# Kernel optimization log

Measured on AMD Instinct MI355X. Metric: run time of the kernel, lower is better.

The kernel has to match this reference:

```python
import jax, jax.numpy as jnp
import numpy as np

B, SX, SL, D, H = 4, 4096, 256, 1024, 16
DH = D // H
LN_EPS = 1e-5
RMS_EPS = 1e-8


def layernorm(x, g, b):
    mu = jnp.mean(x, axis=-1, keepdims=True)
    var = jnp.mean(jnp.square(x - mu), axis=-1, keepdims=True)
    return (x - mu) * jax.lax.rsqrt(var + LN_EPS) * g + b


def rmsnorm(x, gamma):
    # torch: norm = ||x||_2 * dim^-0.5 ; x / clamp(norm, eps) * gamma
    norm = jnp.sqrt(jnp.sum(jnp.square(x), axis=-1, keepdims=True)) * (DH ** -0.5)
    return x / jnp.maximum(norm, RMS_EPS) * gamma


def setup_inputs() -> dict:
    key = jax.random.key(0)
    ks = jax.random.split(key, 6)
    s = 0.02
    return {
        "x": jax.random.normal(ks[0], (B, SX, D), jnp.float32),
        "latents": jax.random.normal(ks[1], (B, SL, D), jnp.float32),
        "mask_x": jnp.ones((B, SX), jnp.float32),
        "mask_latent": jnp.ones((B, SL), jnp.float32),
        "ln_x_g": jnp.ones((D,), jnp.float32),
        "ln_x_b": jnp.zeros((D,), jnp.float32),
        "ln_l_g": jnp.ones((D,), jnp.float32),
        "ln_l_b": jnp.zeros((D,), jnp.float32),
        "Wq": jax.random.normal(ks[2], (D, D), jnp.float32) * s,
        "Wkv": jax.random.normal(ks[3], (D, 2 * D), jnp.float32) * s,
        "qk_gamma": jnp.ones((DH,), jnp.float32),
        "Wo": jax.random.normal(ks[4], (D, D), jnp.float32) * s,
    }


def reference(x, latents, mask_x, mask_latent, ln_x_g, ln_x_b, ln_l_g, ln_l_b, Wq, Wkv, qk_gamma, Wo):
    xn = layernorm(x, ln_x_g, ln_x_b)                       # [B,SX,D]
    ln = layernorm(latents, ln_l_g, ln_l_b)                 # [B,SL,D]

    q = (ln @ Wq).reshape(B, SL, H, DH).transpose(0, 2, 1, 3)      # [B,H,SL,DH]
    kv_in = jnp.concatenate([xn, ln], axis=1)                      # [B,SX+SL,D]
    kv = kv_in @ Wkv
    Skv = SX + SL
    k = kv[..., :D].reshape(B, Skv, H, DH).transpose(0, 2, 1, 3)   # [B,H,Skv,DH]
    v = kv[..., D:].reshape(B, Skv, H, DH).transpose(0, 2, 1, 3)

    # NOTE: original code applies query_norm to BOTH q and k (faithful to source)
    q = rmsnorm(q, qk_gamma)
    k = rmsnorm(k, qk_gamma)

    scores = jnp.einsum("bhqd,bhkd->bhqk", q, k) / np.sqrt(DH)     # [B,H,SL,Skv]

    kv_mask = jnp.concatenate([mask_x, mask_latent], axis=1)       # [B,Skv]
    mask = kv_mask[:, None, :] * mask_latent[:, :, None]           # [B,SL,Skv]
    add_mask = (1.0 - mask)[:, None, :, :] * jnp.finfo(scores.dtype).min
    attn = jax.nn.softmax(scores + add_mask, axis=-1)

    y = jnp.einsum("bhqk,bhkd->bhqd", attn, v)                     # [B,H,SL,DH]
    y = y.transpose(0, 2, 1, 3).reshape(B, SL, D)
    return y @ Wo
```

## Files before the change

### kernel.cpp

```cpp
#include <hip/hip_runtime.h>

#define NB   4
#define SXX  4096
#define SLL  256
#define DD   1024
#define HH   16
#define DHH  64
#define SKV  4352
#define MKV  17408
#define NSPLIT 8

typedef __attribute__((ext_vector_type(8))) short bfrag;
typedef __attribute__((ext_vector_type(4))) float facc;

__device__ __forceinline__ unsigned short f2bf(float f){
  unsigned u = __builtin_bit_cast(unsigned, f);
  u = (u + 0x7fffu + ((u >> 16) & 1u)) >> 16;
  return (unsigned short)u;
}
__device__ __forceinline__ float bf2f(unsigned short h){
  unsigned u = ((unsigned)h) << 16;
  return __builtin_bit_cast(float, u);
}

#define GLOAD_LDS16(g, lds) __builtin_amdgcn_global_load_lds( \
    (const __attribute__((address_space(1))) unsigned int*)(const void*)(g), \
    (__attribute__((address_space(3))) unsigned int*)(void*)(lds), 16, 0, 0)

__global__ void wtrans3(const float* __restrict__ Wq, const float* __restrict__ Wkv,
                        const float* __restrict__ Wo, unsigned short* __restrict__ wqt,
                        unsigned short* __restrict__ wkvt, unsigned short* __restrict__ wot){
  __shared__ float t[32][33];
  int z = blockIdx.z;
  const float* in; unsigned short* out; int N;
  if (z == 0){ in = Wq;  out = wqt;  N = DD;   }
  else if (z == 1){ in = Wkv; out = wkvt; N = 2*DD; }
  else { in = Wo;  out = wot;  N = DD;   }
  int n0 = blockIdx.x * 32, k0 = blockIdx.y * 32;
  if (n0 >= N) return;
  int tx = threadIdx.x, ty = threadIdx.y;
  #pragma unroll
  for (int i = 0; i < 4; i++)
    t[ty + 8*i][tx] = in[(size_t)(k0 + ty + 8*i) * N + n0 + tx];
  __syncthreads();
  #pragma unroll
  for (int i = 0; i < 4; i++)
    out[(size_t)(n0 + ty + 8*i) * DD + k0 + tx] = f2bf(t[tx][ty + 8*i]);
}

__global__ void lnorm(const float* __restrict__ src, const float* __restrict__ g,
                      const float* __restrict__ bt, unsigned short* __restrict__ kvin,
                      unsigned short* __restrict__ dst2, int seq, int off){
  int row = blockIdx.x;
  int b = row / seq, s = row - b*seq;
  int t = threadIdx.x;
  const float4* rp = (const float4*)(src + (size_t)row * DD);
  float4 v = rp[t];
  float sum = v.x + v.y + v.z + v.w;
  float sq  = v.x*v.x + v.y*v.y + v.z*v.z + v.w*v.w;
  #pragma unroll
  for (int o = 32; o > 0; o >>= 1){ sum += __shfl_down(sum, o); sq += __shfl_down(sq, o); }
  __shared__ float ls[8];
  int w = t >> 6, l = t & 63;
  if (l == 0){ ls[w] = sum; ls[4 + w] = sq; }
  __syncthreads();
  sum = ls[0] + ls[1] + ls[2] + ls[3];
  sq  = ls[4] + ls[5] + ls[6] + ls[7];
  float mu  = sum * (1.f/DD);
  float var = sq * (1.f/DD) - mu*mu;
  float rs  = rsqrtf(var + 1e-5f);
  float4 gv = ((const float4*)g)[t];
  float4 bv = ((const float4*)bt)[t];
  ushort4 o4;
  o4.x = f2bf((v.x - mu)*rs*gv.x + bv.x);
  o4.y = f2bf((v.y - mu)*rs*gv.y + bv.y);
  o4.z = f2bf((v.z - mu)*rs*gv.z + bv.z);
  o4.w = f2bf((v.w - mu)*rs*gv.w + bv.w);
  *(ushort4*)(kvin + (size_t)(b*SKV + off + s) * DD + t*4) = o4;
  if (dst2) *(ushort4*)(dst2 + (size_t)row * DD + t*4) = o4;
}

__global__ __launch_bounds__(256) void gemm64(const unsigned short* __restrict__ A,
    const unsigned short* __restrict__ Bt, int M, int N, int K, float* __restrict__ outF){
  __shared__ unsigned short lA[64][72];
  __shared__ unsigned short lB[64][72];
  int n0 = blockIdx.x * 64, m0 = blockIdx.y * 64;
  int t = threadIdx.x, w = t >> 6, l = t & 63;
  int wr = (w >> 1) * 32, wc = (w & 1) * 32;
  int lr = l & 15, kq = (l >> 4) * 8;
  facc acc00 = (facc)0.f, acc01 = (facc)0.f, acc10 = (facc)0.f, acc11 = (facc)0.f;
  for (int k0 = 0; k0 < K; k0 += 64){
    #pragma unroll
    for (int cc = 0; cc < 2; cc++){
      int ch = t + cc*256;
      int row = ch >> 3, cg = (ch & 7) * 8;
      *(bfrag*)&lA[row][cg] = *(const bfrag*)&A[(size_t)(m0 + row) * K + k0 + cg];
      *(bfrag*)&lB[row][cg] = *(const bfrag*)&Bt[(size_t)(n0 + row) * K + k0 + cg];
    }
    __syncthreads();
    #pragma unroll
    for (int ks = 0; ks < 2; ks++){
      bfrag a0 = *(const bfrag*)&lA[wr + lr][ks*32 + kq];
      bfrag a1 = *(const bfrag*)&lA[wr + 16 + lr][ks*32 + kq];
      bfrag b0 = *(const bfrag*)&lB[wc + lr][ks*32 + kq];
      bfrag b1 = *(const bfrag*)&lB[wc + 16 + lr][ks*32 + kq];
      acc00 = __builtin_amdgcn_mfma_f32_16x16x32_bf16(a0, b0, acc00, 0, 0, 0);
      acc01 = __builtin_amdgcn_mfma_f32_16x16x32_bf16(a0, b1, acc01, 0, 0, 0);
      acc10 = __builtin_amdgcn_mfma_f32_16x16x32_bf16(a1, b0, acc10, 0, 0, 0);
      acc11 = __builtin_amdgcn_mfma_f32_16x16x32_bf16(a1, b1, acc11, 0, 0, 0);
    }
    __syncthreads();
  }
  int rl = (l >> 4) * 4, cl = l & 15;
  facc accs[2][2] = {{acc00, acc01},{acc10, acc11}};
  #pragma unroll
  for (int mt = 0; mt < 2; mt++)
  #pragma unroll
  for (int nt = 0; nt < 2; nt++)
  #pragma unroll
  for (int j = 0; j < 4; j++){
    int r = m0 + wr + mt*16 + rl + j;
    int c = n0 + wc + nt*16 + cl;
    outF[(size_t)r * N + c] = accs[mt][nt][j];
  }
}

__global__ __launch_bounds__(256) void gemm_q(const unsigned short* __restrict__ A,
    const unsigned short* __restrict__ Bt, const float* __restrict__ gamma,
    unsigned short* __restrict__ qn){
  __shared__ char smemb[18432];
  unsigned short* lA = (unsigned short*)smemb;
  unsigned short* lB = lA + 64*72;
  float* Cf = (float*)smemb;
  int h = blockIdx.x, n0 = h * 64, m0 = blockIdx.y * 64;
  int t = threadIdx.x, w = t >> 6, l = t & 63;
  int wr = (w >> 1) * 32, wc = (w & 1) * 32;
  int lr = l & 15, kq = (l >> 4) * 8;
  facc acc00 = (facc)0.f, acc01 = (facc)0.f, acc10 = (facc)0.f, acc11 = (facc)0.f;
  for (int k0 = 0; k0 < 1024; k0 += 64){
    #pragma unroll
    for (int cc = 0; cc < 2; cc++){
      int ch = t + cc*256;
      int row = ch >> 3, cg = (ch & 7) * 8;
      *(bfrag*)&lA[row*72 + cg] = *(const bfrag*)&A[(size_t)(m0 + row) * 1024 + k0 + cg];
      *(bfrag*)&lB[row*72 + cg] = *(const bfrag*)&Bt[(size_t)(n0 + row) * 1024 + k0 + cg];
    }
    __syncthreads();
    #pragma unroll
    for (int ks = 0; ks < 2; ks++){
      bfrag a0 = *(const bfrag*)&lA[(wr + lr)*72 + ks*32 + kq];
      bfrag a1 = *(const bfrag*)&lA[(wr + 16 + lr)*72 + ks*32 + kq];
      bfrag b0 = *(const bfrag*)&lB[(wc + lr)*72 + ks*32 + kq];
      bfrag b1 = *(const bfrag*)&lB[(wc + 16 + lr)*72 + ks*32 + kq];
      acc00 = __builtin_amdgcn_mfma_f32_16x16x32_bf16(a0, b0, acc00, 0, 0, 0);
      acc01 = __builtin_amdgcn_mfma_f32_16x16x32_bf16(a0, b1, acc01, 0, 0, 0);
      acc10 = __builtin_amdgcn_mfma_f32_16x16x32_bf16(a1, b0, acc10, 0, 0, 0);
      acc11 = __builtin_amdgcn_mfma_f32_16x16x32_bf16(a1, b1, acc11, 0, 0, 0);
    }
    __syncthreads();
  }
  int rl = (l >> 4) * 4, cl = l & 15;
  facc accs[2][2] = {{acc00, acc01},{acc10, acc11}};
  #pragma unroll
  for (int mt = 0; mt < 2; mt++)
  #pragma unroll
  for (int nt = 0; nt < 2; nt++)
  #pragma unroll
  for (int j = 0; j < 4; j++)
    Cf[(wr + mt*16 + rl + j)*66 + wc + nt*16 + cl] = accs[mt][nt][j];
  __syncthreads();
  if (t < 64){
    const float* src = &Cf[t*66];
    float ss = 0.f;
    #pragma unroll
    for (int d = 0; d < 64; d++){ float a = src[d]; ss = fmaf(a, a, ss); }
    float rv = 0.125f / fmaxf(sqrtf(ss) * 0.125f, 1e-8f);
    int r = m0 + t, b = r >> 8, sl = r & 255;
    unsigned short* dst = &qn[((size_t)(b*HH + h)*SLL + sl)*DHH];
    #pragma unroll
    for (int i = 0; i < 8; i++){
      ushort4 p; float g;
      g = gamma[i*8+0]; p.x = f2bf(src[i*8+0]*g*g*rv);
      g = gamma[i*8+1]; p.y = f2bf(src[i*8+1]*g*g*rv);
      g = gamma[i*8+2]; p.z = f2bf(src[i*8+2]*g*g*rv);
      g = gamma[i*8+3]; p.w = f2bf(src[i*8+3]*g*g*rv);
      ushort4 q;
      g = gamma[i*8+4]; q.x = f2bf(src[i*8+4]*g*g*rv);
      g = gamma[i*8+5]; q.y = f2bf(src[i*8+5]*g*g*rv);
      g = gamma[i*8+6]; q.z = f2bf(src[i*8+6]*g*g*rv);
      g = gamma[i*8+7]; q.w = f2bf(src[i*8+7]*g*g*rv);
      *(ushort4*)&dst[i*8]     = p;
      *(ushort4*)&dst[i*8 + 4] = q;
    }
  }
}

__global__ __launch_bounds__(512, 2) void gemm_kv(const unsigned short* __restrict__ A,
    const unsigned short* __restrict__ Bt,
    const float* __restrict__ mask_x, const float* __restrict__ mask_lat,
    unsigned short* __restrict__ outK, unsigned short* __restrict__ outV,
    float* __restrict__ rkm){
  __shared__ alignas(16) unsigned short lds[3 * 24576];
  int bid = blockIdx.x;
  int wg = (bid & 7) * 136 + (bid >> 3);
  int m0 = (wg >> 4) * 256, n0 = (wg & 15) * 128;
  int t = threadIdx.x, w = t >> 6, l = t & 63;
  int wm = w >> 1, wn = w & 1;
  int lr = l & 15, q2 = l >> 4;
  int r8 = l >> 3, u = l & 7;
  int swz = (u ^ (r8 & 7)) * 8;
  const unsigned short* Ag = A  + (size_t)(m0 + w*8 + r8) * 1024 + swz;
  const unsigned short* Bg = Bt + (size_t)(n0 + w*8 + r8) * 1024 + swz;

  facc acc[4][4];
  #pragma unroll
  for (int mt = 0; mt < 4; mt++)
  #pragma unroll
  for (int nt = 0; nt < 4; nt++) acc[mt][nt] = (facc)0.f;

#define SBAR __builtin_amdgcn_sched_barrier(0)
#define KV_BARRIER do { SBAR; __builtin_amdgcn_s_barrier(); SBAR; } while(0)
#define KV_STA(j, i) GLOAD_LDS16(Ag + (size_t)(i)*65536 + (j)*64, \
    &lds[((j) % 3)*24576 + (i)*4096 + w*512])
#define KV_STB(j, i) GLOAD_LDS16(Bg + (size_t)(i)*65536 + (j)*64, \
    &lds[((j) % 3)*24576 + 16384 + (i)*4096 + w*512])
#define KV_LDFRAG(j, ks) { \
    const unsigned short* pA = &lds[((j) % 3)*24576 + (wm*64 + lr)*64 + (((ks)*4 + q2) ^ (lr & 7))*8]; \
    const unsigned short* pB = &lds[((j) % 3)*24576 + 16384 + (wn*64 + lr)*64 + (((ks)*4 + q2) ^ (lr & 7))*8]; \
    av[0] = *(const bfrag*)(pA);        av[1] = *(const bfrag*)(pA + 1024); \
    av[2] = *(const bfrag*)(pA + 2048); av[3] = *(const bfrag*)(pA + 3072); \
    bv[0] = *(const bfrag*)(pB);        bv[1] = *(const bfrag*)(pB + 1024); \
    bv[2] = *(const bfrag*)(pB + 2048); bv[3] = *(const bfrag*)(pB + 3072); }
#define KV_MFMA do { \
    __builtin_amdgcn_s_setprio(1); \
    _Pragma("unroll") \
    for (int mt = 0; mt < 4; mt++){ \
      _Pragma("unroll") \
      for (int nt = 0; nt < 4; nt++) \
        acc[mt][nt] = __builtin_amdgcn_mfma_f32_16x16x32_bf16(av[mt], bv[nt], acc[mt][nt], 0, 0, 0); } \
    __builtin_amdgcn_s_setprio(0); } while(0)

  KV_STA(0,0); KV_STA(0,1); KV_STA(0,2); KV_STA(0,3); KV_STB(0,0); KV_STB(0,1);
  KV_STA(1,0); KV_STA(1,1); KV_STA(1,2); KV_STA(1,3); KV_STB(1,0); KV_STB(1,1);
  __asm__ volatile("s_waitcnt vmcnt(6)" ::: "memory");
  KV_BARRIER;

  bfrag av[4], bv[4];
  #pragma unroll
  for (int j = 0; j < 16; j++){
    KV_LDFRAG(j, 0);
    if (j < 14){ KV_STA(j+2, 0); KV_STA(j+2, 1); KV_STB(j+2, 0); }
    KV_BARRIER;
    KV_MFMA;
    KV_BARRIER;
    KV_LDFRAG(j, 1);
    if (j < 14){ KV_STA(j+2, 2); KV_STA(j+2, 3); KV_STB(j+2, 1); }
    KV_BARRIER;
    KV_MFMA;
    if (j < 14)       { __asm__ volatile("s_waitcnt vmcnt(6)" ::: "memory"); }
    else if (j == 14) { __asm__ volatile("s_waitcnt vmcnt(0)" ::: "memory"); }
    KV_BARRIER;
  }
#undef KV_STA
#undef KV_STB
#undef KV_LDFRAG
#undef KV_MFMA

  int b = m0 / SKV, s0 = m0 - b*SKV;
  if (n0 < DD){
    #pragma unroll
    for (int mt = 0; mt < 4; mt++)
    #pragma unroll
    for (int nt = 0; nt < 4; nt++)
    #pragma unroll
    for (int j = 0; j < 4; j++)
      lds[(wm*64 + mt*16 + q2*4 + j)*136 + wn*64 + nt*16 + lr] = f2bf(acc[mt][nt][j]);
    __syncthreads();
    int s = t >> 1, hf = t & 1;
    int srow = s0 + s;
    float cm = (srow < SXX) ? mask_x[b*SXX + srow] : mask_lat[b*SLL + srow - SXX];
    const unsigned short* src = &lds[s*136 + hf*64];
    uint4 wv[8];
    #pragma unroll
    for (int i = 0; i < 8; i++) wv[i] = *(const uint4*)&src[i*8];
    float ss0 = 0.f, ss1 = 0.f;
    #pragma unroll
    for (int i = 0; i < 8; i++){
      const unsigned short* pp = (const unsigned short*)&wv[i];
      #pragma unroll
      for (int e = 0; e < 4; e++){
        float a = bf2f(pp[e]);     ss0 = fmaf(a, a, ss0);
        float c = bf2f(pp[e + 4]); ss1 = fmaf(c, c, ss1);
      }
    }
    float rv = 1.f / fmaxf(sqrtf(ss0 + ss1) * 0.125f, 1e-8f);
    int h = (n0 >> 6) + hf;
    unsigned short* dst = &outK[((size_t)(b*HH + h)*SKV + srow)*DHH];
    #pragma unroll
    for (int i = 0; i < 8; i++)
      *(uint4*)&dst[i*8] = wv[i];
    rkm[((size_t)(b*HH + h))*SKV + srow] = (cm != 0.f) ? rv : -1.f;
  } else {
    #pragma unroll
    for (int mt = 0; mt < 4; mt++)
    #pragma unroll
    for (int nt = 0; nt < 4; nt++){
      ushort4 p;
      p.x = f2bf(acc[mt][nt][0]); p.y = f2bf(acc[mt][nt][1]);
      p.z = f2bf(acc[mt][nt][2]); p.w = f2bf(acc[mt][nt][3]);
      *(ushort4*)&lds[(wn*64 + nt*16 + lr)*264 + wm*64 + mt*16 + q2*4] = p;
    }
    __syncthreads();
    int c = t >> 2, sq = t & 3;
    int hh = ((n0 - DD) >> 6) + (c >> 6), d = c & 63;
    const unsigned short* src = &lds[c*264 + sq*64];
    unsigned short* dst = &outV[((size_t)(b*HH + hh)*DHH + d)*SKV + s0 + sq*64];
    #pragma unroll
    for (int i = 0; i < 8; i++)
      *(uint4*)&dst[i*8] = *(const uint4*)&src[i*8];
  }
}

__global__ __launch_bounds__(256) void attn(const unsigned short* __restrict__ qn,
    const unsigned short* __restrict__ kbuf, const unsigned short* __restrict__ vT,
    const float* __restrict__ rkm, const float* __restrict__ mask_lat,
    float* __restrict__ Opart, float* __restrict__ lpart){
  int qt = blockIdx.x, bh = blockIdx.y, split = blockIdx.z;
  int b = bh >> 4;
  __shared__ unsigned short lP[4][2][16][68];
  int t = threadIdx.x, w = t >> 6, l = t & 63;
  int lr = l & 15, q2 = l >> 4, kq = q2 * 8;
  int q0 = qt * 128;
  bfrag aq0[2], aq1[2];
  float rm[2][4];
  #pragma unroll
  for (int tt = 0; tt < 2; tt++){
    const unsigned short* qbase = qn + ((size_t)bh * SLL + q0 + tt*64 + w*16 + lr) * DHH;
    aq0[tt] = *(const bfrag*)&qbase[kq];
    aq1[tt] = *(const bfrag*)&qbase[32 + kq];
    #pragma unroll
    for (int j = 0; j < 4; j++) rm[tt][j] = mask_lat[b*SLL + q0 + tt*64 + w*16 + q2*4 + j];
  }
  facc O[2][4];
  #pragma unroll
  for (int tt = 0; tt < 2; tt++)
  #pragma unroll
  for (int nt = 0; nt < 4; nt++) O[tt][nt] = (facc)0.f;
  float lsum[2][4];
  #pragma unroll
  for (int tt = 0; tt < 2; tt++)
  #pragma unroll
  for (int j = 0; j < 4; j++) lsum[tt][j] = 0.f;

  int t0 = (split * 68) / NSPLIT, t1 = ((split + 1) * 68) / NSPLIT;
  for (int kt = t0; kt < t1; kt++){
    int key0 = kt * 64;
    const unsigned short* kb = kbuf + ((size_t)bh * SKV + key0) * DHH;
    bfrag bk0[4], bk1[4]; float rk[4];
    #pragma unroll
    for (int nt = 0; nt < 4; nt++){
      bk0[nt] = *(const bfrag*)&kb[(nt*16 + lr)*DHH + kq];
      bk1[nt] = *(const bfrag*)&kb[(nt*16 + lr)*DHH + 32 + kq];
      rk[nt]  = rkm[(size_t)bh*SKV + key0 + nt*16 + lr];
    }
    facc S[2][4];
    #pragma unroll
    for (int tt = 0; tt < 2; tt++)
    #pragma unroll
    for (int nt = 0; nt < 4; nt++){
      S[tt][nt] = (facc)0.f;
      S[tt][nt] = __builtin_amdgcn_mfma_f32_16x16x32_bf16(aq0[tt], bk0[nt], S[tt][nt], 0, 0, 0);
      S[tt][nt] = __builtin_amdgcn_mfma_f32_16x16x32_bf16(aq1[tt], bk1[nt], S[tt][nt], 0, 0, 0);
    }
    const unsigned short* vb = vT + (size_t)bh * DHH * SKV + key0;
    bfrag bv0[4], bv1[4];
    #pragma unroll
    for (int nt = 0; nt < 4; nt++){
      bv0[nt] = *(const bfrag*)&vb[(size_t)(nt*16 + lr)*SKV + kq];
      bv1[nt] = *(const bfrag*)&vb[(size_t)(nt*16 + lr)*SKV + 32 + kq];
    }
    #pragma unroll
    for (int tt = 0; tt < 2; tt++){
      #pragma unroll
      for (int j = 0; j < 4; j++){
        float rs_ = 0.f;
        #pragma unroll
        for (int nt = 0; nt < 4; nt++){
          float x = S[tt][nt][j] * rk[nt];
          float sv = (rk[nt] >= 0.f && rm[tt][j] != 0.f) ? x : -3.0e38f;
          float p = __expf(sv - 8.0f);
          rs_ += p;
          lP[w][tt][q2*4 + j][nt*16 + lr] = f2bf(p);
        }
        lsum[tt][j] += rs_;
      }
    }
    __asm__ volatile("s_waitcnt lgkmcnt(0)" ::: "memory");
    bfrag ap0[2], ap1[2];
    #pragma unroll
    for (int tt = 0; tt < 2; tt++){
      ap0[tt] = *(const bfrag*)&lP[w][tt][lr][kq];
      ap1[tt] = *(const bfrag*)&lP[w][tt][lr][32 + kq];
    }
    #pragma unroll
    for (int nt = 0; nt < 4; nt++){
      #pragma unroll
      for (int tt = 0; tt < 2; tt++){
        O[tt][nt] = __builtin_amdgcn_mfma_f32_16x16x32_bf16(ap0[tt], bv0[nt], O[tt][nt], 0, 0, 0);
        O[tt][nt] = __builtin_amdgcn_mfma_f32_16x16x32_bf16(ap1[tt], bv1[nt], O[tt][nt], 0, 0, 0);
      }
    }
  }
  #pragma unroll
  for (int tt = 0; tt < 2; tt++)
  #pragma unroll
  for (int j = 0; j < 4; j++){
    float L = lsum[tt][j];
    L += __shfl_xor(L, 1); L += __shfl_xor(L, 2);
    L += __shfl_xor(L, 4); L += __shfl_xor(L, 8);
    int srow = q0 + tt*64 + w*16 + q2*4 + j;
    size_t obase = (((size_t)split*64 + bh)*SLL + srow)*DHH;
    #pragma unroll
    for (int nt = 0; nt < 4; nt++)
      Opart[obase + nt*16 + lr] = O[tt][nt][j];
    if (lr == 0)
      lpart[((size_t)split*64 + bh)*SLL + srow] = L;
  }
}

__global__ __launch_bounds__(256) void attn_combine(const float* __restrict__ Opart,
    const float* __restrict__ lpart, unsigned short* __restrict__ ybuf){
  int t = threadIdx.x, w = t >> 6, l = t & 63;
  int idx = blockIdx.x * 4 + w;
  int bh = idx >> 8, srow = idx & 255;
  int b = bh >> 4, h = bh & 15;
  float L = 0.f, acc = 0.f;
  #pragma unroll
  for (int s = 0; s < NSPLIT; s++){
    L   += lpart[((size_t)s*64 + bh)*SLL + srow];
    acc += Opart[(((size_t)s*64 + bh)*SLL + srow)*DHH + l];
  }
  ybuf[((size_t)b*SLL + srow)*DD + h*DHH + l] = f2bf(acc / L);
}

extern "C" void kernel_launch(void* const* d_in, const int* in_sizes, int n_in,
                              void* d_out, int out_size, void* d_ws, size_t ws_size,
                              hipStream_t stream) {
  const float* x        = (const float*)d_in[0];
  const float* latents  = (const float*)d_in[1];
  const float* mask_x   = (const float*)d_in[2];
  const float* mask_lat = (const float*)d_in[3];
  const float* ln_x_g   = (const float*)d_in[4];
  const float* ln_x_b   = (const float*)d_in[5];
  const float* ln_l_g   = (const float*)d_in[6];
  const float* ln_l_b   = (const float*)d_in[7];
  const float* Wq       = (const float*)d_in[8];
  const float* Wkv      = (const float*)d_in[9];
  const float* qk_gamma = (const float*)d_in[10];
  const float* Wo       = (const float*)d_in[11];
  float* out = (float*)d_out;

  char* wsb = (char*)d_ws;
  unsigned short* kvin  = (unsigned short*)(wsb + 0);
  unsigned short* lnlat = (unsigned short*)(wsb + 35651584);
  unsigned short* wqt   = (unsigned short*)(wsb + 37748736);
  unsigned short* wkvt  = (unsigned short*)(wsb + 39845888);
  unsigned short* wot   = (unsigned short*)(wsb + 44040192);
  unsigned short* qnb   = (unsigned short*)(wsb + 50331648);
  unsigned short* kbuf  = (unsigned short*)(wsb + 52428800);
  unsigned short* vT    = (unsigned short*)(wsb + 88080384);
  float*          rkm   = (float*)(wsb + 123731968);
  unsigned short* ybuf  = (unsigned short*)(wsb + 124846080);
  float*          Opart = (float*)(wsb + 0);
  float*          lpart = (float*)(wsb + 35651584);

  wtrans3<<<dim3(64, 32, 3), dim3(32, 8), 0, stream>>>(Wq, Wkv, Wo, wqt, wkvt, wot);

  lnorm<<<NB*SXX, 256, 0, stream>>>(x,       ln_x_g, ln_x_b, kvin, nullptr, SXX, 0);
  lnorm<<<NB*SLL, 256, 0, stream>>>(latents, ln_l_g, ln_l_b, kvin, lnlat,   SLL, SXX);

  gemm_q<<<dim3(16, 16), 256, 0, stream>>>(lnlat, wqt, qk_gamma, qnb);
  gemm_kv<<<dim3(1088), 512, 0, stream>>>(kvin, wkvt, mask_x, mask_lat, kbuf, vT, rkm);

  attn<<<dim3(SLL/128, NB*HH, NSPLIT), 256, 0, stream>>>(qnb, kbuf, vT, rkm, mask_lat, Opart, lpart);
  attn_combine<<<(NB*HH*SLL)/4, 256, 0, stream>>>(Opart, lpart, ybuf);

  gemm64<<<dim3(DD/64, (NB*SLL)/64), 256, 0, stream>>>(ybuf, wot, NB*SLL, DD, DD, out);
}
```

Before: 369.1 us.

## Double-buffer LDS fragments in KV GEMM main loop to overlap loads with MFMA

```diff
diff --git a/kernel.cpp b/kernel.cpp
--- a/kernel.cpp
+++ b/kernel.cpp
@@ -224,20 +224,20 @@
     &lds[((j) % 3)*24576 + (i)*4096 + w*512])
 #define KV_STB(j, i) GLOAD_LDS16(Bg + (size_t)(i)*65536 + (j)*64, \
     &lds[((j) % 3)*24576 + 16384 + (i)*4096 + w*512])
-#define KV_LDFRAG(j, ks) { \
+#define KV_LDF(va, vb, j, ks) { \
     const unsigned short* pA = &lds[((j) % 3)*24576 + (wm*64 + lr)*64 + (((ks)*4 + q2) ^ (lr & 7))*8]; \
     const unsigned short* pB = &lds[((j) % 3)*24576 + 16384 + (wn*64 + lr)*64 + (((ks)*4 + q2) ^ (lr & 7))*8]; \
-    av[0] = *(const bfrag*)(pA);        av[1] = *(const bfrag*)(pA + 1024); \
-    av[2] = *(const bfrag*)(pA + 2048); av[3] = *(const bfrag*)(pA + 3072); \
-    bv[0] = *(const bfrag*)(pB);        bv[1] = *(const bfrag*)(pB + 1024); \
-    bv[2] = *(const bfrag*)(pB + 2048); bv[3] = *(const bfrag*)(pB + 3072); }
-#define KV_MFMA do { \
+    va[0] = *(const bfrag*)(pA);        va[1] = *(const bfrag*)(pA + 1024); \
+    va[2] = *(const bfrag*)(pA + 2048); va[3] = *(const bfrag*)(pA + 3072); \
+    vb[0] = *(const bfrag*)(pB);        vb[1] = *(const bfrag*)(pB + 1024); \
+    vb[2] = *(const bfrag*)(pB + 2048); vb[3] = *(const bfrag*)(pB + 3072); }
+#define KV_MFMA(va, vb) do { \
     __builtin_amdgcn_s_setprio(1); \
     _Pragma("unroll") \
     for (int mt = 0; mt < 4; mt++){ \
       _Pragma("unroll") \
       for (int nt = 0; nt < 4; nt++) \
-        acc[mt][nt] = __builtin_amdgcn_mfma_f32_16x16x32_bf16(av[mt], bv[nt], acc[mt][nt], 0, 0, 0); } \
+        acc[mt][nt] = __builtin_amdgcn_mfma_f32_16x16x32_bf16(va[mt], vb[nt], acc[mt][nt], 0, 0, 0); } \
     __builtin_amdgcn_s_setprio(0); } while(0)
 
   KV_STA(0,0); KV_STA(0,1); KV_STA(0,2); KV_STA(0,3); KV_STB(0,0); KV_STB(0,1);
@@ -245,25 +245,31 @@
   __asm__ volatile("s_waitcnt vmcnt(6)" ::: "memory");
   KV_BARRIER;
 
-  bfrag av[4], bv[4];
+  bfrag avA[4], bvA[4], avB[4], bvB[4];
+  KV_LDF(avA, bvA, 0, 0);
   #pragma unroll
   for (int j = 0; j < 16; j++){
-    KV_LDFRAG(j, 0);
+    KV_LDF(avB, bvB, j, 1);
     if (j < 14){ KV_STA(j+2, 0); KV_STA(j+2, 1); KV_STB(j+2, 0); }
-    KV_BARRIER;
-    KV_MFMA;
-    KV_BARRIER;
-    KV_LDFRAG(j, 1);
-    if (j < 14){ KV_STA(j+2, 2); KV_STA(j+2, 3); KV_STB(j+2, 1); }
-    KV_BARRIER;
-    KV_MFMA;
-    if (j < 14)       { __asm__ volatile("s_waitcnt vmcnt(6)" ::: "memory"); }
+    SBAR;
+    __asm__ volatile("s_waitcnt lgkmcnt(8)" ::: "memory");
+    SBAR;
+    KV_MFMA(avA, bvA);
+    if (j < 14)       { __asm__ volatile("s_waitcnt vmcnt(3)" ::: "memory"); }
     else if (j == 14) { __asm__ volatile("s_waitcnt vmcnt(0)" ::: "memory"); }
     KV_BARRIER;
+    if (j < 15) KV_LDF(avA, bvA, j+1, 0);
+    if (j < 14){ KV_STA(j+2, 2); KV_STA(j+2, 3); KV_STB(j+2, 1); }
+    SBAR;
+    if (j < 15) { __asm__ volatile("s_waitcnt lgkmcnt(8)" ::: "memory"); }
+    else        { __asm__ volatile("s_waitcnt lgkmcnt(0)" ::: "memory"); }
+    SBAR;
+    KV_MFMA(avB, bvB);
+    KV_BARRIER;
   }
 #undef KV_STA
 #undef KV_STB
-#undef KV_LDFRAG
+#undef KV_LDF
 #undef KV_MFMA
 
   int b = m0 / SKV, s0 = m0 - b*SKV;
```

Result: no change. 375.9 us (+1.8%).
